# Optimization experiments

Measured on AMD Instinct MI355X. Metric: run time of the kernel, lower is better.

The kernel has to match this reference:

```python
import jax, jax.numpy as jnp
import numpy as np

A, B, C, D, DT, STEPS = 0.02, 0.2, -65.0, 8.0, 1.0, 100
H, I, O = 8192, 4096, 4096


def _compress(x, gain):
    return jnp.sign(x) * jnp.log1p(gain * jnp.abs(x) + 1e-6)


def setup_inputs() -> dict:
    key = jax.random.key(0)
    k1, k2, k3, k4, k5 = jax.random.split(key, 5)
    return {
        "v_input": jax.random.normal(k1, (I,), jnp.float32),
        "target_output": jax.random.normal(k2, (O,), jnp.float32),
        "W1": jax.random.uniform(k3, (H, I), jnp.float32) * 0.05,
        "W2": jax.random.uniform(k4, (O, H), jnp.float32) * 0.05,
        "W_feedback": jax.random.uniform(k5, (H, O), jnp.float32) * 0.02,
        "gain1": jnp.float32(1.0),
        "gain2": jnp.float32(1.0),
    }


def reference(v_input, target_output, W1, W2, W_feedback, gain1, gain2):
    # Input currents are loop-invariant in the original torch loop; compute once.
    I_hidden = _compress(W1 @ v_input, gain1)            # [H]
    I_output = _compress(W2 @ I_hidden, gain2)           # [O]
    I_hidden = I_hidden - W_feedback @ I_output          # [H]
    total_input = jnp.concatenate([I_hidden, I_output])  # [H+O]

    n = total_input.shape[0]
    v0 = jnp.full((n,), -65.0, jnp.float32)
    u0 = B * v0

    def step(carry, _):
        v_prev, u_prev = carry
        v = v_prev + DT * (0.04 * v_prev ** 2 + 5.0 * v_prev + 0.14 - u_prev + total_input)
        u = u_prev + DT * A * (B * v_prev - u_prev)
        spiked = v >= 30.0
        v = jnp.where(spiked, C, v)
        u = jnp.where(spiked, u + D, u)
        return (v, u), (v, u)

    _, (vs, us) = jax.lax.scan(step, (v0, u0), None, length=STEPS - 1)
    v_vec = jnp.concatenate([v0[None, :], vs], axis=0)  # [STEPS, H+O]
    u_vec = jnp.concatenate([u0[None, :], us], axis=0)

    loss = jnp.mean((I_output - target_output) ** 2)
    return loss, v_vec, u_vec
```

## Files before the change

### kernel.cpp

```cpp
#include <hip/hip_runtime.h>
#include <math.h>

#define HSZ 8192
#define ISZ 4096
#define OSZ 4096
#define NTOT (HSZ + OSZ)
#define STEPS 100

__device__ __forceinline__ float bf2f(unsigned short h) {
    union { unsigned u; float f; } c; c.u = ((unsigned)h) << 16; return c.f;
}

__device__ __forceinline__ double compress_d(double x, double gain) {
    double s = (x > 0.0) ? 1.0 : ((x < 0.0) ? -1.0 : 0.0);
    return s * log1p(gain * fabs(x) + 1e-6);
}

__device__ __forceinline__ double wred(double a) {
    #pragma unroll
    for (int o = 32; o > 0; o >>= 1) a += __shfl_down(a, o, 64);
    return a;
}

__global__ void detect_kernel(const void* W1, int* flag) {
    if (threadIdx.x == 0 && blockIdx.x == 0) {
        const unsigned short* p = (const unsigned short*)W1;
        int bf = 1;
        for (int i = 0; i < 128; ++i) {
            unsigned short a = (unsigned short)(p[i] & 0x7FFF);
            if (a > 0x3D80) bf = 0;
        }
        *flag = bf;
    }
}

template <int C, int XIN>
__global__ void mv_compress(const void* __restrict__ W, const void* __restrict__ x,
                            const void* __restrict__ gain, float* __restrict__ y,
                            const int* __restrict__ flag) {
    const int wave = threadIdx.x >> 6, lane = threadIdx.x & 63;
    const int row = blockIdx.x * 4 + wave;
    const int bf = *flag;
    double acc = 0.0;
    if (bf) {
        const ushort4* Wr = (const ushort4*)((const unsigned short*)W + (size_t)row * C);
        if (XIN) {
            const ushort4* xv = (const ushort4*)x;
            for (int it = 0; it < C / 256; ++it) {
                const int i = it * 64 + lane;
                ushort4 w = Wr[i], xx = xv[i];
                acc += (double)bf2f(w.x) * (double)bf2f(xx.x);
                acc += (double)bf2f(w.y) * (double)bf2f(xx.y);
                acc += (double)bf2f(w.z) * (double)bf2f(xx.z);
                acc += (double)bf2f(w.w) * (double)bf2f(xx.w);
            }
        } else {
            const float4* xv = (const float4*)x;
            for (int it = 0; it < C / 256; ++it) {
                const int i = it * 64 + lane;
                ushort4 w = Wr[i]; float4 xx = xv[i];
                acc += (double)bf2f(w.x) * (double)xx.x;
                acc += (double)bf2f(w.y) * (double)xx.y;
                acc += (double)bf2f(w.z) * (double)xx.z;
                acc += (double)bf2f(w.w) * (double)xx.w;
            }
        }
    } else {
        const float4* Wr = (const float4*)((const float*)W + (size_t)row * C);
        const float4* xv = (const float4*)x;
        for (int it = 0; it < C / 256; ++it) {
            const int i = it * 64 + lane;
            float4 w = Wr[i], xx = xv[i];
            acc += (double)w.x * (double)xx.x;
            acc += (double)w.y * (double)xx.y;
            acc += (double)w.z * (double)xx.z;
            acc += (double)w.w * (double)xx.w;
        }
    }
    acc = wred(acc);
    if (lane == 0) {
        float g = bf ? bf2f(*(const unsigned short*)gain) : *(const float*)gain;
        y[row] = (float)compress_d(acc, (double)g);
    }
}

__global__ void mv_feedback(const void* __restrict__ Wfb, const float* __restrict__ io,
                            const float* __restrict__ h1c, float* __restrict__ hid,
                            const int* __restrict__ flag) {
    const int wave = threadIdx.x >> 6, lane = threadIdx.x & 63;
    const int row = blockIdx.x * 4 + wave;
    const int bf = *flag;
    double acc = 0.0;
    const float4* xv = (const float4*)io;
    if (bf) {
        const ushort4* Wr = (const ushort4*)((const unsigned short*)Wfb + (size_t)row * OSZ);
        for (int it = 0; it < OSZ / 256; ++it) {
            const int i = it * 64 + lane;
            ushort4 w = Wr[i]; float4 xx = xv[i];
            acc += (double)bf2f(w.x) * (double)xx.x;
            acc += (double)bf2f(w.y) * (double)xx.y;
            acc += (double)bf2f(w.z) * (double)xx.z;
            acc += (double)bf2f(w.w) * (double)xx.w;
        }
    } else {
        const float4* Wr = (const float4*)((const float*)Wfb + (size_t)row * OSZ);
        for (int it = 0; it < OSZ / 256; ++it) {
            const int i = it * 64 + lane;
            float4 w = Wr[i], xx = xv[i];
            acc += (double)w.x * (double)xx.x;
            acc += (double)w.y * (double)xx.y;
            acc += (double)w.z * (double)xx.z;
            acc += (double)w.w * (double)xx.w;
        }
    }
    acc = wred(acc);
    if (lane == 0) hid[row] = h1c[row] - (float)acc;
}

__global__ void loss_kernel(const float* __restrict__ io, const void* __restrict__ tgt,
                            float* __restrict__ out, const int* __restrict__ flag) {
    __shared__ double red[4];
    const int bf = *flag;
    double acc = 0.0;
    for (int i = threadIdx.x; i < OSZ; i += 256) {
        float t = bf ? bf2f(((const unsigned short*)tgt)[i]) : ((const float*)tgt)[i];
        double d = (double)io[i] - (double)t;
        acc += d * d;
    }
    acc = wred(acc);
    if ((threadIdx.x & 63) == 0) red[threadIdx.x >> 6] = acc;
    __syncthreads();
    if (threadIdx.x == 0)
        out[0] = (float)((red[0] + red[1] + red[2] + red[3]) / (double)OSZ);
}

__global__ void sim_kernel(const float* __restrict__ hid, const float* __restrict__ io,
                           float* __restrict__ vout, float* __restrict__ uout) {
    const int n = blockIdx.x * blockDim.x + threadIdx.x;
    if (n >= NTOT) return;
    const float ti = (n < HSZ) ? hid[n] : io[n - HSZ];
    float v = -65.0f;
    float u = 0.2f * v;
    vout[n] = v;
    uout[n] = u;
    for (int s = 1; s < STEPS; ++s) {
        float dv = 0.04f * (v * v);
        dv = dv + 5.0f * v;
        dv = dv + 0.14f;
        dv = dv - u;
        dv = dv + ti;
        float vn = v + 1.0f * dv;
        float du = 0.2f * v - u;
        float un = u + 0.02f * du;
        bool sp = (vn >= 30.0f);
        v = sp ? -65.0f : vn;
        u = sp ? (un + 8.0f) : un;
        vout[(size_t)s * NTOT + n] = v;
        uout[(size_t)s * NTOT + n] = u;
    }
}

extern "C" void kernel_launch(void* const* d_in, const int* in_sizes, int n_in,
                              void* d_out, int out_size, void* d_ws, size_t ws_size,
                              hipStream_t stream) {
    const void* v_input = d_in[0];
    const void* target  = d_in[1];
    const void* W1      = d_in[2];
    const void* W2      = d_in[3];
    const void* Wfb     = d_in[4];
    const void* gain1   = d_in[5];
    const void* gain2   = d_in[6];

    float* out  = (float*)d_out;
    float* vout = out + 1;
    float* uout = out + 1 + (size_t)STEPS * NTOT;

    int*   flag = (int*)d_ws;
    float* base = (float*)((char*)d_ws + 256);
    float* h1c  = base;
    float* io   = base + HSZ;
    float* hid  = io + OSZ;

    detect_kernel<<<1, 64, 0, stream>>>(W1, flag);
    mv_compress<ISZ, 1><<<HSZ / 4, 256, 0, stream>>>(W1, v_input, gain1, h1c, flag);
    mv_compress<HSZ, 0><<<OSZ / 4, 256, 0, stream>>>(W2, h1c, gain2, io, flag);
    mv_feedback<<<HSZ / 4, 256, 0, stream>>>(Wfb, io, h1c, hid, flag);
    loss_kernel<<<1, 256, 0, stream>>>(io, target, out, flag);
    sim_kernel<<<NTOT / 256, 256, 0, stream>>>(hid, io, vout, uout);
}
```

Before: 384.6 us.

## Inline dtype detection, widen matvec loads, fuse loss into sim kernel

Drops the separate detect kernel and has every block detect bf16 inputs with a wave ballot. The three matvec kernels become one templated kernel that uses one 256-thread block per row with 16-byte vector loads and an unrolled loop. The loss computation moves into an extra block of the simulation kernel. Together these cut the launch count from six to four and widen memory accesses, at the cost of redundant detection reads in every block and a shared-memory reduction per row.

Result: faster. 364.9 us (-5.1%).

```diff
diff --git a/kernel.cpp b/kernel.cpp
--- a/kernel.cpp
+++ b/kernel.cpp
@@ -6,6 +6,8 @@
 #define OSZ 4096
 #define NTOT (HSZ + OSZ)
 #define STEPS 100
+
+typedef unsigned short ushort8v __attribute__((ext_vector_type(8)));
 
 __device__ __forceinline__ float bf2f(unsigned short h) {
     union { unsigned u; float f; } c; c.u = ((unsigned)h) << 16; return c.f;
@@ -22,54 +24,59 @@
     return a;
 }
 
-__global__ void detect_kernel(const void* W1, int* flag) {
-    if (threadIdx.x == 0 && blockIdx.x == 0) {
-        const unsigned short* p = (const unsigned short*)W1;
-        int bf = 1;
-        for (int i = 0; i < 128; ++i) {
-            unsigned short a = (unsigned short)(p[i] & 0x7FFF);
-            if (a > 0x3D80) bf = 0;
-        }
-        *flag = bf;
-    }
+__device__ __forceinline__ int detect_bf(const void* W1) {
+    const unsigned short* p = (const unsigned short*)W1;
+    const int lane = threadIdx.x & 63;
+    const unsigned short a0 = (unsigned short)(p[lane] & 0x7FFF);
+    const unsigned short a1 = (unsigned short)(p[64 + lane] & 0x7FFF);
+    unsigned long long bad = __ballot((a0 > 0x3D80) || (a1 > 0x3D80));
+    return bad == 0ull;
 }
 
-template <int C, int XIN>
-__global__ void mv_compress(const void* __restrict__ W, const void* __restrict__ x,
-                            const void* __restrict__ gain, float* __restrict__ y,
-                            const int* __restrict__ flag) {
-    const int wave = threadIdx.x >> 6, lane = threadIdx.x & 63;
-    const int row = blockIdx.x * 4 + wave;
-    const int bf = *flag;
+template <int K, int XIN, int DOCOMP>
+__global__ __launch_bounds__(256) void mv_kernel(
+        const void* __restrict__ W, const void* __restrict__ x,
+        const void* __restrict__ gain, const float* __restrict__ base,
+        float* __restrict__ y, const void* __restrict__ Wdet) {
+    const int bf = detect_bf(Wdet);
+    const int row = blockIdx.x;
+    const int t = threadIdx.x;
     double acc = 0.0;
     if (bf) {
-        const ushort4* Wr = (const ushort4*)((const unsigned short*)W + (size_t)row * C);
+        const ushort8v* Wr = (const ushort8v*)((const unsigned short*)W + (size_t)row * K);
         if (XIN) {
-            const ushort4* xv = (const ushort4*)x;
-            for (int it = 0; it < C / 256; ++it) {
-                const int i = it * 64 + lane;
-                ushort4 w = Wr[i], xx = xv[i];
-                acc += (double)bf2f(w.x) * (double)bf2f(xx.x);
-                acc += (double)bf2f(w.y) * (double)bf2f(xx.y);
-                acc += (double)bf2f(w.z) * (double)bf2f(xx.z);
-                acc += (double)bf2f(w.w) * (double)bf2f(xx.w);
+            const ushort8v* xv = (const ushort8v*)x;
+            #pragma unroll
+            for (int c = 0; c < K / 2048; ++c) {
+                const int i = c * 256 + t;
+                ushort8v w = Wr[i], xx = xv[i];
+                #pragma unroll
+                for (int j = 0; j < 8; ++j)
+                    acc += (double)bf2f(w[j]) * (double)bf2f(xx[j]);
             }
         } else {
             const float4* xv = (const float4*)x;
-            for (int it = 0; it < C / 256; ++it) {
-                const int i = it * 64 + lane;
-                ushort4 w = Wr[i]; float4 xx = xv[i];
-                acc += (double)bf2f(w.x) * (double)xx.x;
-                acc += (double)bf2f(w.y) * (double)xx.y;
-                acc += (double)bf2f(w.z) * (double)xx.z;
-                acc += (double)bf2f(w.w) * (double)xx.w;
+            #pragma unroll
+            for (int c = 0; c < K / 2048; ++c) {
+                const int i = c * 256 + t;
+                ushort8v w = Wr[i];
+                float4 x0 = xv[2 * i], x1 = xv[2 * i + 1];
+                acc += (double)bf2f(w[0]) * (double)x0.x;
+                acc += (double)bf2f(w[1]) * (double)x0.y;
+                acc += (double)bf2f(w[2]) * (double)x0.z;
+                acc += (double)bf2f(w[3]) * (double)x0.w;
+                acc += (double)bf2f(w[4]) * (double)x1.x;
+                acc += (double)bf2f(w[5]) * (double)x1.y;
+                acc += (double)bf2f(w[6]) * (double)x1.z;
+                acc += (double)bf2f(w[7]) * (double)x1.w;
             }
         }
     } else {
-        const float4* Wr = (const float4*)((const float*)W + (size_t)row * C);
+        const float4* Wr = (const float4*)((const float*)W + (size_t)row * K);
         const float4* xv = (const float4*)x;
-        for (int it = 0; it < C / 256; ++it) {
-            const int i = it * 64 + lane;
+        #pragma unroll
+        for (int c = 0; c < K / 1024; ++c) {
+            const int i = c * 256 + t;
             float4 w = Wr[i], xx = xv[i];
             acc += (double)w.x * (double)xx.x;
             acc += (double)w.y * (double)xx.y;
@@ -78,69 +85,46 @@
         }
     }
     acc = wred(acc);
-    if (lane == 0) {
-        float g = bf ? bf2f(*(const unsigned short*)gain) : *(const float*)gain;
-        y[row] = (float)compress_d(acc, (double)g);
+    __shared__ double red[4];
+    if ((t & 63) == 0) red[t >> 6] = acc;
+    __syncthreads();
+    if (t == 0) {
+        const double s = red[0] + red[1] + red[2] + red[3];
+        if (DOCOMP) {
+            const float g = bf ? bf2f(*(const unsigned short*)gain) : *(const float*)gain;
+            y[row] = (float)compress_d(s, (double)g);
+        } else {
+            y[row] = base[row] - (float)s;
+        }
     }
 }
 
-__global__ void mv_feedback(const void* __restrict__ Wfb, const float* __restrict__ io,
-                            const float* __restrict__ h1c, float* __restrict__ hid,
-                            const int* __restrict__ flag) {
-    const int wave = threadIdx.x >> 6, lane = threadIdx.x & 63;
-    const int row = blockIdx.x * 4 + wave;
-    const int bf = *flag;
-    double acc = 0.0;
-    const float4* xv = (const float4*)io;
-    if (bf) {
-        const ushort4* Wr = (const ushort4*)((const unsigned short*)Wfb + (size_t)row * OSZ);
-        for (int it = 0; it < OSZ / 256; ++it) {
-            const int i = it * 64 + lane;
-            ushort4 w = Wr[i]; float4 xx = xv[i];
-            acc += (double)bf2f(w.x) * (double)xx.x;
-            acc += (double)bf2f(w.y) * (double)xx.y;
-            acc += (double)bf2f(w.z) * (double)xx.z;
-            acc += (double)bf2f(w.w) * (double)xx.w;
+__global__ __launch_bounds__(256) void sim_loss_kernel(
+        const float* __restrict__ hid, const float* __restrict__ io,
+        const void* __restrict__ tgt, float* __restrict__ loss_out,
+        float* __restrict__ vout, float* __restrict__ uout,
+        const void* __restrict__ Wdet) {
+    if (blockIdx.x == NTOT / 256) {
+        const int bf = detect_bf(Wdet);
+        __shared__ double red[4];
+        double acc = 0.0;
+        for (int i = threadIdx.x; i < OSZ; i += 256) {
+            const float tv = bf ? bf2f(((const unsigned short*)tgt)[i])
+                                : ((const float*)tgt)[i];
+            const double d = (double)io[i] - (double)tv;
+            acc += d * d;
         }
-    } else {
-        const float4* Wr = (const float4*)((const float*)Wfb + (size_t)row * OSZ);
-        for (int it = 0; it < OSZ / 256; ++it) {
-            const int i = it * 64 + lane;
-            float4 w = Wr[i], xx = xv[i];
-            acc += (double)w.x * (double)xx.x;
-            acc += (double)w.y * (double)xx.y;
-            acc += (double)w.z * (double)xx.z;
-            acc += (double)w.w * (double)xx.w;
-        }
+        acc = wred(acc);
+        if ((threadIdx.x & 63) == 0) red[threadIdx.x >> 6] = acc;
+        __syncthreads();
+        if (threadIdx.x == 0)
+            loss_out[0] = (float)((red[0] + red[1] + red[2] + red[3]) / (double)OSZ);
+        return;
     }
-    acc = wred(acc);
-    if (lane == 0) hid[row] = h1c[row] - (float)acc;
-}
-
-__global__ void loss_kernel(const float* __restrict__ io, const void* __restrict__ tgt,
-                            float* __restrict__ out, const int* __restrict__ flag) {
-    __shared__ double red[4];
-    const int bf = *flag;
-    double acc = 0.0;
-    for (int i = threadIdx.x; i < OSZ; i += 256) {
-        float t = bf ? bf2f(((const unsigned short*)tgt)[i]) : ((const float*)tgt)[i];
-        double d = (double)io[i] - (double)t;
-        acc += d * d;
-    }
-    acc = wred(acc);
-    if ((threadIdx.x & 63) == 0) red[threadIdx.x >> 6] = acc;
-    __syncthreads();
-    if (threadIdx.x == 0)
-        out[0] = (float)((red[0] + red[1] + red[2] + red[3]) / (double)OSZ);
-}
-
-__global__ void sim_kernel(const float* __restrict__ hid, const float* __restrict__ io,
-                           float* __restrict__ vout, float* __restrict__ uout) {
-    const int n = blockIdx.x * blockDim.x + threadIdx.x;
-    if (n >= NTOT) return;
+    const int n = blockIdx.x * 256 + threadIdx.x;
     const float ti = (n < HSZ) ? hid[n] : io[n - HSZ];
     float v = -65.0f;
-    float u = 0.2f * v;
+    float u = -13.0f;
     vout[n] = v;
     uout[n] = u;
     for (int s = 1; s < STEPS; ++s) {
@@ -175,16 +159,12 @@
     float* vout = out + 1;
     float* uout = out + 1 + (size_t)STEPS * NTOT;
 
-    int*   flag = (int*)d_ws;
-    float* base = (float*)((char*)d_ws + 256);
-    float* h1c  = base;
-    float* io   = base + HSZ;
-    float* hid  = io + OSZ;
+    float* h1c = (float*)d_ws;
+    float* io  = h1c + HSZ;
+    float* hid = io + OSZ;
 
-    detect_kernel<<<1, 64, 0, stream>>>(W1, flag);
-    mv_compress<ISZ, 1><<<HSZ / 4, 256, 0, stream>>>(W1, v_input, gain1, h1c, flag);
-    mv_compress<HSZ, 0><<<OSZ / 4, 256, 0, stream>>>(W2, h1c, gain2, io, flag);
-    mv_feedback<<<HSZ / 4, 256, 0, stream>>>(Wfb, io, h1c, hid, flag);
-    loss_kernel<<<1, 256, 0, stream>>>(io, target, out, flag);
-    sim_kernel<<<NTOT / 256, 256, 0, stream>>>(hid, io, vout, uout);
+    mv_kernel<ISZ, 1, 1><<<HSZ, 256, 0, stream>>>(W1, v_input, gain1, nullptr, h1c, W1);
+    mv_kernel<HSZ, 0, 1><<<OSZ, 256, 0, stream>>>(W2, h1c, gain2, nullptr, io, W1);
+    mv_kernel<OSZ, 0, 0><<<HSZ, 256, 0, stream>>>(Wfb, io, nullptr, h1c, hid, W1);
+    sim_loss_kernel<<<NTOT / 256 + 1, 256, 0, stream>>>(hid, io, target, out, vout, uout, W1);
 }
```
